# Kernel tuning notes

Hardware: AMD Instinct MI355X
Metric: run time of the kernel (lower is better)

The kernel has to match this reference:

```python
import jax, jax.numpy as jnp
import numpy as np

T = 16          # time_span
N = 128         # num_trajectory
D = 512         # embedding dim
TEMP = 0.1      # temperature
INF = 1000000000.0
M = 2 * N * T   # total rows of z (two views)


def setup_inputs() -> dict:
    key = jax.random.key(0)
    k1, k2 = jax.random.split(key)
    z = jax.random.normal(k1, (M, D), dtype=jnp.float32)
    done = jax.random.randint(k2, (T, N), 0, 2).astype(jnp.int32)  # [T, N] binary done flags
    return {"z": z, "done": done}


def _build_positive_mask(done):
    # done: [T, N] int -> transposed to [N, T] as in the torch code
    d = done.astype(jnp.float32).T  # [N, T]
    # Sequential rewrite loop is equivalent to:
    #   done_new[r,t] = 1 iff exists original done at p < t in row r AND orig done[r,t] == 0
    excl = jnp.cumsum(d, axis=1) - d  # exclusive cumsum along time
    d_new = jnp.where((excl > 0) & (d == 0), 1.0, 0.0)  # [N, T]
    done_vec = 1.0 - d_new.reshape(-1)  # [N*T]
    # block-diagonal temporal mask: same trajectory => 1
    traj = jnp.arange(N * T) // T
    block = (traj[:, None] == traj[None, :]).astype(jnp.float32)  # [NT, NT]
    done_mask = (done_vec[:, None] * done_vec[None, :]) * block
    done_mask = jnp.tile(done_mask, (2, 2))      # [M, M]
    temporal_mask = jnp.tile(block, (2, 2))      # [M, M]
    eye = jnp.eye(M, dtype=jnp.float32)
    positive_mask = (1.0 - done_mask) * (1.0 - temporal_mask) + eye
    return positive_mask, eye


def reference(z, done):
    positive_mask, eye = _build_positive_mask(done)
    # cosine similarity = normalize + GEMM (same math as broadcasted F.cosine_similarity)
    norms = jnp.maximum(jnp.linalg.norm(z, axis=-1, keepdims=True), 1e-8)
    zn = z / norms
    logits = (zn @ zn.T) / TEMP - eye * INF  # [M, M]
    log_probs = jax.nn.log_softmax(logits, axis=1)
    neg = 1.0 - positive_mask
    mean_log_prob = jnp.sum(neg * log_probs, axis=1) / jnp.sum(neg, axis=1)
    return -jnp.mean(mean_log_prob)
```

## Files before the change

### kernel.cpp

```cpp
#include <hip/hip_runtime.h>
#include <hip/hip_bf16.h>

typedef __bf16 bf16x8 __attribute__((ext_vector_type(8)));
typedef float f32x16 __attribute__((ext_vector_type(16)));
typedef unsigned int u32x4 __attribute__((ext_vector_type(4)));
typedef unsigned short u16;


__global__ void nrm_kernel(const float* __restrict__ z, u16* __restrict__ zn,
                           float* __restrict__ expsum, float* __restrict__ possum) {
    int row = blockIdx.x;
    int tid = threadIdx.x;
    float4 v = ((const float4*)(z + row * 512))[tid];
    float ss = v.x * v.x + v.y * v.y + v.z * v.z + v.w * v.w;
#pragma unroll
    for (int off = 32; off; off >>= 1) ss += __shfl_down(ss, off, 64);
    __shared__ float red[2];
    if ((tid & 63) == 0) red[tid >> 6] = ss;
    __syncthreads();
    float norm = fmaxf(sqrtf(red[0] + red[1]), 1e-8f);
    float sc = 1.0f / norm;
    __hip_bfloat16 b[4];
    b[0] = __float2bfloat16(v.x * sc);
    b[1] = __float2bfloat16(v.y * sc);
    b[2] = __float2bfloat16(v.z * sc);
    b[3] = __float2bfloat16(v.w * sc);
    uint2 p;
    __builtin_memcpy(&p, b, 8);
    ((uint2*)(zn + row * 512))[tid] = p;
    if (tid == 0) { expsum[row] = 0.f; possum[row] = 0.f; }
}

__global__ void pos_kernel(const u16* __restrict__ zn, float* __restrict__ possum) {
    int g = blockIdx.x;
    int l = threadIdx.x;
    int u = l & 31, h = l >> 5;
    int grow = (u < 16) ? (g * 16 + u) : (2048 + g * 16 + (u - 16));
    const u32x4* src = (const u32x4*)(zn + grow * 512);
    f32x16 acc = {};
#pragma unroll
    for (int kc = 0; kc < 32; ++kc) {
        bf16x8 f = __builtin_bit_cast(bf16x8, src[h + 2 * kc]);
        acc = __builtin_amdgcn_mfma_f32_32x32x16_bf16(f, f, acc, 0, 0, 0);
    }
#pragma unroll
    for (int r = 0; r < 16; ++r) {
        int rrow = (r & 3) + 8 * (r >> 2) + 4 * h;
        float v = (rrow == u) ? 0.f : acc[r];
        v += __shfl_xor(v, 1, 64);
        v += __shfl_xor(v, 2, 64);
        v += __shfl_xor(v, 4, 64);
        v += __shfl_xor(v, 8, 64);
        v += __shfl_xor(v, 16, 64);
        if (u == 0) {
            int gr = (rrow < 16) ? (g * 16 + rrow) : (2048 + g * 16 + (rrow - 16));
            possum[gr] = v * 10.0f;
        }
    }
}

__global__ __launch_bounds__(256, 2) void gemm_kernel(const u16* __restrict__ zn,
                                                      float* __restrict__ expsum) {
    __shared__ u16 Bt[32 * 520];
    int wave = threadIdx.x >> 6;
    int l = threadIdx.x & 63;
    int m = l & 31, h = l >> 5;
    int rowbase = blockIdx.x * 128 + wave * 32;
    int colchunk = blockIdx.y * 256;

    u32x4 a[32];
    const u32x4* arow = (const u32x4*)(zn + (rowbase + m) * 512);
#pragma unroll
    for (int kc = 0; kc < 32; ++kc) a[kc] = arow[h + 2 * kc];

    float expacc[16];
#pragma unroll
    for (int r = 0; r < 16; ++r) expacc[r] = 0.f;

    int c = threadIdx.x >> 3;
    int g0 = threadIdx.x & 7;

    for (int ct = 0; ct < 8; ++ct) {
        int colbase = colchunk + ct * 32;
        __syncthreads();
        const u32x4* src = (const u32x4*)(zn + (colbase + c) * 512);
        u32x4* dst = (u32x4*)(Bt + c * 520);
#pragma unroll
        for (int i = 0; i < 8; ++i) dst[g0 + 8 * i] = src[g0 + 8 * i];
        __syncthreads();

        f32x16 acc = {};
        const u32x4* brow = (const u32x4*)(Bt + m * 520);
#pragma unroll
        for (int kc = 0; kc < 32; ++kc) {
            bf16x8 bf = __builtin_bit_cast(bf16x8, brow[h + 2 * kc]);
            acc = __builtin_amdgcn_mfma_f32_32x32x16_bf16(
                __builtin_bit_cast(bf16x8, a[kc]), bf, acc, 0, 0, 0);
        }
        if (colbase == rowbase) {
#pragma unroll
            for (int r = 0; r < 16; ++r) {
                int rrow = (r & 3) + 8 * (r >> 2) + 4 * h;
                if (rrow != m) expacc[r] += __expf(acc[r] * 10.0f);
            }
        } else {
#pragma unroll
            for (int r = 0; r < 16; ++r) expacc[r] += __expf(acc[r] * 10.0f);
        }
    }
#pragma unroll
    for (int r = 0; r < 16; ++r) {
        float v = expacc[r];
        v += __shfl_xor(v, 1, 64);
        v += __shfl_xor(v, 2, 64);
        v += __shfl_xor(v, 4, 64);
        v += __shfl_xor(v, 8, 64);
        v += __shfl_xor(v, 16, 64);
        if (m == 0) {
            int rrow = (r & 3) + 8 * (r >> 2) + 4 * h;
            atomicAdd(&expsum[rowbase + rrow], v);
        }
    }
}

__global__ void fin_kernel(const float* __restrict__ expsum,
                           const float* __restrict__ possum, float* __restrict__ out) {
    int tid = threadIdx.x;
    float s = 0.f;
    for (int i = tid; i < 4096; i += 1024)
        s += __logf(expsum[i]) - possum[i] * (1.0f / 31.0f);
#pragma unroll
    for (int off = 32; off; off >>= 1) s += __shfl_down(s, off, 64);
    __shared__ float red[16];
    if ((tid & 63) == 0) red[tid >> 6] = s;
    __syncthreads();
    if (tid == 0) {
        float t = 0.f;
#pragma unroll
        for (int i = 0; i < 16; ++i) t += red[i];
        out[0] = t * (1.0f / 4096.0f);
    }
}

extern "C" void kernel_launch(void* const* d_in, const int* in_sizes, int n_in,
                              void* d_out, int out_size, void* d_ws, size_t ws_size,
                              hipStream_t stream) {
    const float* z = (const float*)d_in[0];
    u16* zn = (u16*)d_ws;
    float* expsum = (float*)((char*)d_ws + (4u << 20));
    float* possum = expsum + 4096;
    float* out = (float*)d_out;

    nrm_kernel<<<4096, 128, 0, stream>>>(z, zn, expsum, possum);
    pos_kernel<<<128, 64, 0, stream>>>(zn, possum);
    gemm_kernel<<<dim3(32, 16), 256, 0, stream>>>(zn, expsum);
    fin_kernel<<<1, 1024, 0, stream>>>(expsum, possum, out);
}
```

Before: 97.42 us.

## Exploit symmetry of similarity matrix, fuse positive-sum kernel, double-buffer swizzled LDS

The GEMM now computes only upper-triangular 128x128 tiles of the symmetric zn·znᵀ matrix. Each tile's exponentials are added to both the row sums and, via per-column atomics, the column sums, which roughly halves MFMA and exp work. The separate positive-sum kernel is merged into the same launch as extra blocks, and the B tile load uses double-buffered LDS with an XOR swizzle, register staging and s_setprio around the MFMA loop. In exchange there are more global atomics, a serial loop to map block index to triangle tile, and higher LDS use per block.

```diff
diff --git a/kernel.cpp b/kernel.cpp
--- a/kernel.cpp
+++ b/kernel.cpp
@@ -31,86 +31,139 @@
     if (tid == 0) { expsum[row] = 0.f; possum[row] = 0.f; }
 }
 
-__global__ void pos_kernel(const u16* __restrict__ zn, float* __restrict__ possum) {
-    int g = blockIdx.x;
-    int l = threadIdx.x;
-    int u = l & 31, h = l >> 5;
-    int grow = (u < 16) ? (g * 16 + u) : (2048 + g * 16 + (u - 16));
-    const u32x4* src = (const u32x4*)(zn + grow * 512);
-    f32x16 acc = {};
-#pragma unroll
-    for (int kc = 0; kc < 32; ++kc) {
-        bf16x8 f = __builtin_bit_cast(bf16x8, src[h + 2 * kc]);
-        acc = __builtin_amdgcn_mfma_f32_32x32x16_bf16(f, f, acc, 0, 0, 0);
-    }
-#pragma unroll
-    for (int r = 0; r < 16; ++r) {
-        int rrow = (r & 3) + 8 * (r >> 2) + 4 * h;
-        float v = (rrow == u) ? 0.f : acc[r];
-        v += __shfl_xor(v, 1, 64);
-        v += __shfl_xor(v, 2, 64);
-        v += __shfl_xor(v, 4, 64);
-        v += __shfl_xor(v, 8, 64);
-        v += __shfl_xor(v, 16, 64);
-        if (u == 0) {
-            int gr = (rrow < 16) ? (g * 16 + rrow) : (2048 + g * 16 + (rrow - 16));
-            possum[gr] = v * 10.0f;
-        }
-    }
-}
-
 __global__ __launch_bounds__(256, 2) void gemm_kernel(const u16* __restrict__ zn,
-                                                      float* __restrict__ expsum) {
-    __shared__ u16 Bt[32 * 520];
+                                                      float* __restrict__ expsum,
+                                                      float* __restrict__ possum) {
+    if (blockIdx.x >= 528) {
+        if (threadIdx.x < 64) {
+            int g = blockIdx.x - 528;
+            int l = threadIdx.x;
+            int u = l & 31, h2 = l >> 5;
+            int grow = (u < 16) ? (g * 16 + u) : (2048 + g * 16 + (u - 16));
+            const u32x4* src = (const u32x4*)(zn + grow * 512);
+            f32x16 acc = {};
+#pragma unroll
+            for (int kc = 0; kc < 32; ++kc) {
+                bf16x8 f = __builtin_bit_cast(bf16x8, src[h2 + 2 * kc]);
+                acc = __builtin_amdgcn_mfma_f32_32x32x16_bf16(f, f, acc, 0, 0, 0);
+            }
+#pragma unroll
+            for (int r = 0; r < 16; ++r) {
+                int rrow = (r & 3) + 8 * (r >> 2) + 4 * h2;
+                float v = (rrow == u) ? 0.f : acc[r];
+                v += __shfl_xor(v, 1, 64);
+                v += __shfl_xor(v, 2, 64);
+                v += __shfl_xor(v, 4, 64);
+                v += __shfl_xor(v, 8, 64);
+                v += __shfl_xor(v, 16, 64);
+                if (u == 0) {
+                    int gr = (rrow < 16) ? (g * 16 + rrow) : (2048 + g * 16 + (rrow - 16));
+                    possum[gr] = v * 10.0f;
+                }
+            }
+        }
+        return;
+    }
+
+    __shared__ u16 Bt[2][32 * 512];
+
+    int b = blockIdx.x;
+    int ti = 0;
+    while (b >= 32 - ti) { b -= 32 - ti; ++ti; }
+    int tj = ti + b;
+
     int wave = threadIdx.x >> 6;
     int l = threadIdx.x & 63;
     int m = l & 31, h = l >> 5;
-    int rowbase = blockIdx.x * 128 + wave * 32;
-    int colchunk = blockIdx.y * 256;
+    int rowbase = ti * 128 + wave * 32;
+    int colbase = tj * 128;
+    bool diag = (ti == tj);
 
     u32x4 a[32];
     const u32x4* arow = (const u32x4*)(zn + (rowbase + m) * 512);
 #pragma unroll
     for (int kc = 0; kc < 32; ++kc) a[kc] = arow[h + 2 * kc];
 
-    float expacc[16];
-#pragma unroll
-    for (int r = 0; r < 16; ++r) expacc[r] = 0.f;
+    float racc[16];
+#pragma unroll
+    for (int r = 0; r < 16; ++r) racc[r] = 0.f;
 
     int c = threadIdx.x >> 3;
     int g0 = threadIdx.x & 7;
-
-    for (int ct = 0; ct < 8; ++ct) {
-        int colbase = colchunk + ct * 32;
-        __syncthreads();
-        const u32x4* src = (const u32x4*)(zn + (colbase + c) * 512);
-        u32x4* dst = (u32x4*)(Bt + c * 520);
-#pragma unroll
-        for (int i = 0; i < 8; ++i) dst[g0 + 8 * i] = src[g0 + 8 * i];
-        __syncthreads();
-
+    int woff = c * 64 + (g0 ^ (c & 7));
+    const u16* zsrc = zn + (colbase + c) * 512;
+
+    u32x4 stg[8];
+    {
+        const u32x4* src = (const u32x4*)zsrc;
+#pragma unroll
+        for (int i = 0; i < 8; ++i) stg[i] = src[g0 + 8 * i];
+        u32x4* dst = ((u32x4*)Bt[0]) + woff;
+#pragma unroll
+        for (int i = 0; i < 8; ++i) dst[8 * i] = stg[i];
+    }
+
+    int sw0 = m & 1, sw12 = (m >> 1) & 3;
+    int rbyte[4];
+#pragma unroll
+    for (int q = 0; q < 4; ++q)
+        rbyte[q] = m * 1024 + (h ^ sw0) * 16 + ((q ^ sw12) * 32);
+
+    const char* rb = (const char*)Bt[0];
+    char* wb = (char*)Bt[1];
+    __syncthreads();
+
+    for (int ct = 0; ct < 4; ++ct) {
+        if (ct < 3) {
+            const u32x4* src = (const u32x4*)(zsrc + (ct + 1) * 32 * 512);
+#pragma unroll
+            for (int i = 0; i < 8; ++i) stg[i] = src[g0 + 8 * i];
+        }
         f32x16 acc = {};
-        const u32x4* brow = (const u32x4*)(Bt + m * 520);
-#pragma unroll
-        for (int kc = 0; kc < 32; ++kc) {
-            bf16x8 bf = __builtin_bit_cast(bf16x8, brow[h + 2 * kc]);
-            acc = __builtin_amdgcn_mfma_f32_32x32x16_bf16(
-                __builtin_bit_cast(bf16x8, a[kc]), bf, acc, 0, 0, 0);
-        }
-        if (colbase == rowbase) {
+        __builtin_amdgcn_s_setprio(1);
+#pragma unroll
+        for (int kg = 0; kg < 8; ++kg) {
+#pragma unroll
+            for (int q = 0; q < 4; ++q) {
+                bf16x8 bf = *(const bf16x8*)(rb + rbyte[q] + kg * 128);
+                acc = __builtin_amdgcn_mfma_f32_32x32x16_bf16(
+                    __builtin_bit_cast(bf16x8, a[4 * kg + q]), bf, acc, 0, 0, 0);
+            }
+        }
+        __builtin_amdgcn_s_setprio(0);
+
+        if (diag && ct == wave) {
 #pragma unroll
             for (int r = 0; r < 16; ++r) {
                 int rrow = (r & 3) + 8 * (r >> 2) + 4 * h;
-                if (rrow != m) expacc[r] += __expf(acc[r] * 10.0f);
+                if (rrow != m) racc[r] += __builtin_exp2f(acc[r] * 14.426950408889634f);
             }
         } else {
-#pragma unroll
-            for (int r = 0; r < 16; ++r) expacc[r] += __expf(acc[r] * 10.0f);
-        }
-    }
+            float csum = 0.f;
+#pragma unroll
+            for (int r = 0; r < 16; ++r) {
+                float e = __builtin_exp2f(acc[r] * 14.426950408889634f);
+                racc[r] += e;
+                csum += e;
+            }
+            if (!diag) {
+                csum += __shfl_xor(csum, 32, 64);
+                if (h == 0) atomicAdd(&expsum[colbase + ct * 32 + m], csum);
+            }
+        }
+
+        if (ct < 3) {
+            u32x4* dst = ((u32x4*)wb) + woff;
+#pragma unroll
+            for (int i = 0; i < 8; ++i) dst[8 * i] = stg[i];
+        }
+        __syncthreads();
+        const char* t = rb; rb = (const char*)wb; wb = (char*)t;
+    }
+
 #pragma unroll
     for (int r = 0; r < 16; ++r) {
-        float v = expacc[r];
+        float v = racc[r];
         v += __shfl_xor(v, 1, 64);
         v += __shfl_xor(v, 2, 64);
         v += __shfl_xor(v, 4, 64);
@@ -152,7 +205,6 @@
     float* out = (float*)d_out;
 
     nrm_kernel<<<4096, 128, 0, stream>>>(z, zn, expsum, possum);
-    pos_kernel<<<128, 64, 0, stream>>>(zn, possum);
-    gemm_kernel<<<dim3(32, 16), 256, 0, stream>>>(zn, expsum);
+    gemm_kernel<<<656, 256, 0, stream>>>(zn, expsum, possum);
     fin_kernel<<<1, 1024, 0, stream>>>(expsum, possum, out);
 }
```

Result: no change. 95.56 us (-1.9%).
